# Kernel optimization log

Measured on AMD Instinct MI355X. Metric: run time of the kernel, lower is better.

## Reference

```python
import jax, jax.numpy as jnp
import numpy as np

B, N, D = 32, 1024, 512

def setup_inputs() -> dict:
    key = jax.random.key(0)
    ks = jax.random.split(key, 5)
    s = 1.0 / np.sqrt(D)
    return {
        "x": jax.random.normal(ks[0], (B, N, D), jnp.float32),
        "Wq": jax.random.normal(ks[1], (D, D), jnp.float32) * s,
        "bq": jnp.zeros((D,), jnp.float32),
        "Wk": jax.random.normal(ks[2], (D, D), jnp.float32) * s,
        "bk": jnp.zeros((D,), jnp.float32),
        "Wv": jax.random.normal(ks[3], (D, D), jnp.float32) * s,
        "bv": jnp.zeros((D,), jnp.float32),
        "pos_bias": jax.random.normal(ks[4], (N, N), jnp.float32) * 0.02,
    }

def reference(x, Wq, bq, Wk, bk, Wv, bv, pos_bias):
    # torch nn.Linear: y = x @ W.T + b
    q = x @ Wq.T + bq                      # [B,N,D]
    k = x @ Wk.T + bk                      # [B,N,D]
    v = x @ Wv.T + bv                      # [B,N,D]
    # AFT-full: out[b,t,d] = sig(q)[b,t,d] * sum_s exp(k[b,s,d]+w[t,s]) v[b,s,d]
    #                                        / sum_s exp(k[b,s,d]+w[t,s])
    # exp(k+w) factors as exp(w)*exp(k); the num/den ratio is invariant to
    # per-row shifts of w and per-(b,d) shifts of k, so stabilize both.
    w = pos_bias - jnp.max(pos_bias, axis=1, keepdims=True)   # [T,S]
    kk = k - jnp.max(k, axis=1, keepdims=True)                # [B,S,D]
    ew = jnp.exp(w)
    ek = jnp.exp(kk)
    num = jnp.einsum('ts,bsd->btd', ew, ek * v)               # [B,T,D]
    den = jnp.einsum('ts,bsd->btd', ew, ek)                   # [B,T,D]
    return jax.nn.sigmoid(q) * (num / den)
```

## Files before the change

### kernel.cpp

```cpp
#include <hip/hip_runtime.h>

typedef unsigned short u16;
typedef unsigned int u32;
using frag8 = __attribute__((ext_vector_type(8))) short;
using f32x4 = __attribute__((ext_vector_type(4))) float;

__device__ __forceinline__ u16 f2bf(float f) {
  union { float f; u32 u; } x;
  x.f = f;
  u32 r = (x.u + 0x7fffu + ((x.u >> 16) & 1u)) >> 16;
  return (u16)r;
}

__device__ __forceinline__ void stage_tile(const u16* g, int ld, u16* lds, int tid) {
  const int wv = tid >> 6;
#pragma unroll
  for (int i = 0; i < 2; ++i) {
    const int c = i * 256 + tid;
    const int row = c >> 2;
    const int col = (c & 3) * 8;
    __builtin_amdgcn_global_load_lds(
        (const __attribute__((address_space(1))) void*)(g + (size_t)row * ld + col),
        (__attribute__((address_space(3))) void*)(lds + (size_t)(i * 256 + wv * 64) * 8),
        16, 0, 0);
  }
}

__global__ void conv_kernel(const float* __restrict__ src, u16* __restrict__ dst, int n4) {
  int i = blockIdx.x * 256 + threadIdx.x;
  if (i >= n4) return;
  float4 v = ((const float4*)src)[i];
  ushort4 o;
  o.x = f2bf(v.x); o.y = f2bf(v.y); o.z = f2bf(v.z); o.w = f2bf(v.w);
  ((ushort4*)dst)[i] = o;
}

__global__ void expw_kernel(const float* __restrict__ src, u16* __restrict__ dst, int n4) {
  int i = blockIdx.x * 256 + threadIdx.x;
  if (i >= n4) return;
  float4 v = ((const float4*)src)[i];
  ushort4 o;
  o.x = f2bf(__expf(v.x)); o.y = f2bf(__expf(v.y));
  o.z = f2bf(__expf(v.z)); o.w = f2bf(__expf(v.w));
  ((ushort4*)dst)[i] = o;
}

__global__ __launch_bounds__(256, 3) void q_kernel(const u16* __restrict__ xb,
                                                   const u16* __restrict__ wqb,
                                                   const float* __restrict__ bq,
                                                   float* __restrict__ out) {
  __shared__ __align__(16) u16 As[128 * 32];
  __shared__ __align__(16) u16 Bs[128 * 32];
  const int tid = threadIdx.x;
  const int lane = tid & 63, wv = tid >> 6;
  const int wm = (wv & 1) * 64, wn = (wv >> 1) * 64;
  const int fr = lane & 15, quad = lane >> 4;
  const int m0 = blockIdx.y * 128;
  const int n0 = blockIdx.x * 128;
  f32x4 acc[4][4] = {};
  for (int k0 = 0; k0 < 512; k0 += 32) {
    stage_tile(xb + (size_t)m0 * 512 + k0, 512, As, tid);
    stage_tile(wqb + (size_t)n0 * 512 + k0, 512, Bs, tid);
    __syncthreads();
    frag8 a[4], b[4];
#pragma unroll
    for (int i = 0; i < 4; ++i) a[i] = *(const frag8*)&As[(wm + i * 16 + fr) * 32 + quad * 8];
#pragma unroll
    for (int i = 0; i < 4; ++i) b[i] = *(const frag8*)&Bs[(wn + i * 16 + fr) * 32 + quad * 8];
#pragma unroll
    for (int mi = 0; mi < 4; ++mi)
#pragma unroll
      for (int ni = 0; ni < 4; ++ni)
        acc[mi][ni] = __builtin_amdgcn_mfma_f32_16x16x32_bf16(a[mi], b[ni], acc[mi][ni], 0, 0, 0);
    __syncthreads();
  }
#pragma unroll
  for (int mi = 0; mi < 4; ++mi)
#pragma unroll
    for (int ni = 0; ni < 4; ++ni) {
      const int col = n0 + wn + ni * 16 + fr;
      const float bqv = bq[col];
#pragma unroll
      for (int r = 0; r < 4; ++r) {
        const int row = m0 + wm + mi * 16 + quad * 4 + r;
        const float qv = acc[mi][ni][r] + bqv;
        out[(size_t)row * 512 + col] = 1.0f / (1.0f + __expf(-qv));
      }
    }
}

__global__ __launch_bounds__(256, 2) void kv_kernel(const u16* __restrict__ xb,
                                                    const u16* __restrict__ wkb,
                                                    const u16* __restrict__ wvb,
                                                    const float* __restrict__ bk,
                                                    const float* __restrict__ bv,
                                                    u16* __restrict__ ekT,
                                                    u16* __restrict__ ekvT) {
  __shared__ __align__(16) u16 Ak[128 * 32];
  __shared__ __align__(16) u16 Av[128 * 32];
  __shared__ __align__(16) u16 Bs[128 * 32];
  const int tid = threadIdx.x;
  const int lane = tid & 63, wv = tid >> 6;
  const int wm = (wv & 1) * 64, wn = (wv >> 1) * 64;
  const int fr = lane & 15, quad = lane >> 4;
  const int s0 = blockIdx.x * 128;
  const int d0 = blockIdx.y * 128;
  const int b  = blockIdx.z;
  f32x4 acck[4][4] = {}, accv[4][4] = {};
  for (int k0 = 0; k0 < 512; k0 += 32) {
    stage_tile(wkb + (size_t)d0 * 512 + k0, 512, Ak, tid);
    stage_tile(wvb + (size_t)d0 * 512 + k0, 512, Av, tid);
    stage_tile(xb + ((size_t)b * 1024 + s0) * 512 + k0, 512, Bs, tid);
    __syncthreads();
    frag8 ak[4], av[4], bb[4];
#pragma unroll
    for (int i = 0; i < 4; ++i) {
      ak[i] = *(const frag8*)&Ak[(wm + i * 16 + fr) * 32 + quad * 8];
      av[i] = *(const frag8*)&Av[(wm + i * 16 + fr) * 32 + quad * 8];
      bb[i] = *(const frag8*)&Bs[(wn + i * 16 + fr) * 32 + quad * 8];
    }
#pragma unroll
    for (int mi = 0; mi < 4; ++mi)
#pragma unroll
      for (int ni = 0; ni < 4; ++ni) {
        acck[mi][ni] = __builtin_amdgcn_mfma_f32_16x16x32_bf16(ak[mi], bb[ni], acck[mi][ni], 0, 0, 0);
        accv[mi][ni] = __builtin_amdgcn_mfma_f32_16x16x32_bf16(av[mi], bb[ni], accv[mi][ni], 0, 0, 0);
      }
    __syncthreads();
  }
#pragma unroll
  for (int mi = 0; mi < 4; ++mi)
#pragma unroll
    for (int r = 0; r < 4; ++r) {
      const int d = d0 + wm + mi * 16 + quad * 4 + r;
      const float bkv = bk[d], bvv = bv[d];
#pragma unroll
      for (int ni = 0; ni < 4; ++ni) {
        const int s = s0 + wn + ni * 16 + fr;
        const float ek = __expf(acck[mi][ni][r] + bkv);
        const float vv = accv[mi][ni][r] + bvv;
        const size_t idx = ((size_t)b * 512 + d) * 1024 + s;
        ekT[idx]  = f2bf(ek);
        ekvT[idx] = f2bf(ek * vv);
      }
    }
}

__global__ __launch_bounds__(256, 2) void aft_kernel(const u16* __restrict__ ew,
                                                     const u16* __restrict__ ekT,
                                                     const u16* __restrict__ ekvT,
                                                     float* __restrict__ out) {
  __shared__ __align__(16) u16 As[128 * 32];
  __shared__ __align__(16) u16 B1[128 * 32];
  __shared__ __align__(16) u16 B2[128 * 32];
  const int tid = threadIdx.x;
  const int lane = tid & 63, wv = tid >> 6;
  const int wm = (wv & 1) * 64, wn = (wv >> 1) * 64;
  const int fr = lane & 15, quad = lane >> 4;
  const int d0 = blockIdx.x * 128;
  const int t0 = blockIdx.y * 128;
  const int b  = blockIdx.z;
  f32x4 accn[4][4] = {}, accd[4][4] = {};
  for (int k0 = 0; k0 < 1024; k0 += 32) {
    stage_tile(ew + (size_t)t0 * 1024 + k0, 1024, As, tid);
    stage_tile(ekvT + ((size_t)b * 512 + d0) * 1024 + k0, 1024, B1, tid);
    stage_tile(ekT + ((size_t)b * 512 + d0) * 1024 + k0, 1024, B2, tid);
    __syncthreads();
    frag8 a[4], b1[4], b2[4];
#pragma unroll
    for (int i = 0; i < 4; ++i) {
      a[i]  = *(const frag8*)&As[(wm + i * 16 + fr) * 32 + quad * 8];
      b1[i] = *(const frag8*)&B1[(wn + i * 16 + fr) * 32 + quad * 8];
      b2[i] = *(const frag8*)&B2[(wn + i * 16 + fr) * 32 + quad * 8];
    }
#pragma unroll
    for (int mi = 0; mi < 4; ++mi)
#pragma unroll
      for (int ni = 0; ni < 4; ++ni) {
        accn[mi][ni] = __builtin_amdgcn_mfma_f32_16x16x32_bf16(a[mi], b1[ni], accn[mi][ni], 0, 0, 0);
        accd[mi][ni] = __builtin_amdgcn_mfma_f32_16x16x32_bf16(a[mi], b2[ni], accd[mi][ni], 0, 0, 0);
      }
    __syncthreads();
  }
#pragma unroll
  for (int mi = 0; mi < 4; ++mi)
#pragma unroll
    for (int ni = 0; ni < 4; ++ni)
#pragma unroll
      for (int r = 0; r < 4; ++r) {
        const int t = t0 + wm + mi * 16 + quad * 4 + r;
        const int d = d0 + wn + ni * 16 + fr;
        const size_t idx = ((size_t)b * 1024 + t) * 512 + d;
        const float sq = out[idx];
        out[idx] = sq * accn[mi][ni][r] / accd[mi][ni][r];
      }
}

extern "C" void kernel_launch(void* const* d_in, const int* in_sizes, int n_in,
                              void* d_out, int out_size, void* d_ws, size_t ws_size,
                              hipStream_t stream) {
  const float* x  = (const float*)d_in[0];
  const float* Wq = (const float*)d_in[1];
  const float* bq = (const float*)d_in[2];
  const float* Wk = (const float*)d_in[3];
  const float* bk = (const float*)d_in[4];
  const float* Wv = (const float*)d_in[5];
  const float* bv = (const float*)d_in[6];
  const float* pb = (const float*)d_in[7];
  float* out = (float*)d_out;
  char* ws = (char*)d_ws;
  u16* xb   = (u16*)(ws);
  u16* wqb  = (u16*)(ws + 33554432);
  u16* wkb  = (u16*)(ws + 34078720);
  u16* wvb  = (u16*)(ws + 34603008);
  u16* ewb  = (u16*)(ws + 35127296);
  u16* ekT  = (u16*)(ws + 37224448);
  u16* ekvT = (u16*)(ws + 70778880);

  conv_kernel<<<16384, 256, 0, stream>>>(x, xb, 16777216 / 4);
  conv_kernel<<<256, 256, 0, stream>>>(Wq, wqb, 262144 / 4);
  conv_kernel<<<256, 256, 0, stream>>>(Wk, wkb, 262144 / 4);
  conv_kernel<<<256, 256, 0, stream>>>(Wv, wvb, 262144 / 4);
  expw_kernel<<<1024, 256, 0, stream>>>(pb, ewb, 1048576 / 4);

  q_kernel<<<dim3(4, 256), 256, 0, stream>>>(xb, wqb, bq, out);
  kv_kernel<<<dim3(8, 4, 32), 256, 0, stream>>>(xb, wkb, wvb, bk, bv, ekT, ekvT);
  aft_kernel<<<dim3(4, 8, 32), 256, 0, stream>>>(ewb, ekT, ekvT, out);
}
```

Measured before the change: 294.7 us.

## Double GEMM K-tile to 64 with XOR-swizzled LDS and merge prep kernels

```diff
diff --git a/kernel.cpp b/kernel.cpp
--- a/kernel.cpp
+++ b/kernel.cpp
@@ -12,36 +12,49 @@
   return (u16)r;
 }
 
-__device__ __forceinline__ void stage_tile(const u16* g, int ld, u16* lds, int tid) {
+__device__ __forceinline__ void stage_tile64(const u16* g, int ld, u16* lds, int tid) {
   const int wv = tid >> 6;
 #pragma unroll
-  for (int i = 0; i < 2; ++i) {
+  for (int i = 0; i < 4; ++i) {
     const int c = i * 256 + tid;
-    const int row = c >> 2;
-    const int col = (c & 3) * 8;
+    const int row = c >> 3;
+    const int colc = (c & 7) ^ (row & 7);
     __builtin_amdgcn_global_load_lds(
-        (const __attribute__((address_space(1))) void*)(g + (size_t)row * ld + col),
+        (const __attribute__((address_space(1))) void*)(g + (size_t)row * ld + colc * 8),
         (__attribute__((address_space(3))) void*)(lds + (size_t)(i * 256 + wv * 64) * 8),
         16, 0, 0);
   }
 }
 
-__global__ void conv_kernel(const float* __restrict__ src, u16* __restrict__ dst, int n4) {
-  int i = blockIdx.x * 256 + threadIdx.x;
-  if (i >= n4) return;
+__device__ __forceinline__ frag8 frag_read64(const u16* lds, int row, int kk, int quad) {
+  const int cc = (kk * 4 + quad) ^ (row & 7);
+  return *(const frag8*)&lds[row * 64 + cc * 8];
+}
+
+__global__ void prep_kernel(const float* __restrict__ x, const float* __restrict__ Wq,
+                            const float* __restrict__ Wk, const float* __restrict__ Wv,
+                            const float* __restrict__ pb, u16* __restrict__ xb,
+                            u16* __restrict__ wqb, u16* __restrict__ wkb,
+                            u16* __restrict__ wvb, u16* __restrict__ ewb) {
+  const int blk = blockIdx.x;
+  const float* src;
+  u16* dst;
+  int base;
+  bool ex = false;
+  if (blk < 16384)      { src = x;  dst = xb;  base = blk; }
+  else if (blk < 16640) { src = Wq; dst = wqb; base = blk - 16384; }
+  else if (blk < 16896) { src = Wk; dst = wkb; base = blk - 16640; }
+  else if (blk < 17152) { src = Wv; dst = wvb; base = blk - 16896; }
+  else                  { src = pb; dst = ewb; base = blk - 17152; ex = true; }
+  const int i = base * 256 + threadIdx.x;
   float4 v = ((const float4*)src)[i];
   ushort4 o;
-  o.x = f2bf(v.x); o.y = f2bf(v.y); o.z = f2bf(v.z); o.w = f2bf(v.w);
-  ((ushort4*)dst)[i] = o;
-}
-
-__global__ void expw_kernel(const float* __restrict__ src, u16* __restrict__ dst, int n4) {
-  int i = blockIdx.x * 256 + threadIdx.x;
-  if (i >= n4) return;
-  float4 v = ((const float4*)src)[i];
-  ushort4 o;
-  o.x = f2bf(__expf(v.x)); o.y = f2bf(__expf(v.y));
-  o.z = f2bf(__expf(v.z)); o.w = f2bf(__expf(v.w));
+  if (ex) {
+    o.x = f2bf(__expf(v.x)); o.y = f2bf(__expf(v.y));
+    o.z = f2bf(__expf(v.z)); o.w = f2bf(__expf(v.w));
+  } else {
+    o.x = f2bf(v.x); o.y = f2bf(v.y); o.z = f2bf(v.z); o.w = f2bf(v.w);
+  }
   ((ushort4*)dst)[i] = o;
 }
 
@@ -49,8 +62,8 @@
                                                    const u16* __restrict__ wqb,
                                                    const float* __restrict__ bq,
                                                    float* __restrict__ out) {
-  __shared__ __align__(16) u16 As[128 * 32];
-  __shared__ __align__(16) u16 Bs[128 * 32];
+  __shared__ __align__(16) u16 As[128 * 64];
+  __shared__ __align__(16) u16 Bs[128 * 64];
   const int tid = threadIdx.x;
   const int lane = tid & 63, wv = tid >> 6;
   const int wm = (wv & 1) * 64, wn = (wv >> 1) * 64;
@@ -58,20 +71,24 @@
   const int m0 = blockIdx.y * 128;
   const int n0 = blockIdx.x * 128;
   f32x4 acc[4][4] = {};
-  for (int k0 = 0; k0 < 512; k0 += 32) {
-    stage_tile(xb + (size_t)m0 * 512 + k0, 512, As, tid);
-    stage_tile(wqb + (size_t)n0 * 512 + k0, 512, Bs, tid);
-    __syncthreads();
-    frag8 a[4], b[4];
-#pragma unroll
-    for (int i = 0; i < 4; ++i) a[i] = *(const frag8*)&As[(wm + i * 16 + fr) * 32 + quad * 8];
-#pragma unroll
-    for (int i = 0; i < 4; ++i) b[i] = *(const frag8*)&Bs[(wn + i * 16 + fr) * 32 + quad * 8];
-#pragma unroll
-    for (int mi = 0; mi < 4; ++mi)
-#pragma unroll
-      for (int ni = 0; ni < 4; ++ni)
-        acc[mi][ni] = __builtin_amdgcn_mfma_f32_16x16x32_bf16(a[mi], b[ni], acc[mi][ni], 0, 0, 0);
+  for (int k0 = 0; k0 < 512; k0 += 64) {
+    stage_tile64(xb + (size_t)m0 * 512 + k0, 512, As, tid);
+    stage_tile64(wqb + (size_t)n0 * 512 + k0, 512, Bs, tid);
+    __syncthreads();
+#pragma unroll
+    for (int kk = 0; kk < 2; ++kk) {
+      frag8 a[4], b[4];
+#pragma unroll
+      for (int i = 0; i < 4; ++i) {
+        a[i] = frag_read64(As, wm + i * 16 + fr, kk, quad);
+        b[i] = frag_read64(Bs, wn + i * 16 + fr, kk, quad);
+      }
+#pragma unroll
+      for (int mi = 0; mi < 4; ++mi)
+#pragma unroll
+        for (int ni = 0; ni < 4; ++ni)
+          acc[mi][ni] = __builtin_amdgcn_mfma_f32_16x16x32_bf16(a[mi], b[ni], acc[mi][ni], 0, 0, 0);
+    }
     __syncthreads();
   }
 #pragma unroll
@@ -96,9 +113,9 @@
                                                     const float* __restrict__ bv,
                                                     u16* __restrict__ ekT,
                                                     u16* __restrict__ ekvT) {
-  __shared__ __align__(16) u16 Ak[128 * 32];
-  __shared__ __align__(16) u16 Av[128 * 32];
-  __shared__ __align__(16) u16 Bs[128 * 32];
+  __shared__ __align__(16) u16 Ak[128 * 64];
+  __shared__ __align__(16) u16 Av[128 * 64];
+  __shared__ __align__(16) u16 Bs[128 * 64];
   const int tid = threadIdx.x;
   const int lane = tid & 63, wv = tid >> 6;
   const int wm = (wv & 1) * 64, wn = (wv >> 1) * 64;
@@ -107,25 +124,28 @@
   const int d0 = blockIdx.y * 128;
   const int b  = blockIdx.z;
   f32x4 acck[4][4] = {}, accv[4][4] = {};
-  for (int k0 = 0; k0 < 512; k0 += 32) {
-    stage_tile(wkb + (size_t)d0 * 512 + k0, 512, Ak, tid);
-    stage_tile(wvb + (size_t)d0 * 512 + k0, 512, Av, tid);
-    stage_tile(xb + ((size_t)b * 1024 + s0) * 512 + k0, 512, Bs, tid);
-    __syncthreads();
-    frag8 ak[4], av[4], bb[4];
-#pragma unroll
-    for (int i = 0; i < 4; ++i) {
-      ak[i] = *(const frag8*)&Ak[(wm + i * 16 + fr) * 32 + quad * 8];
-      av[i] = *(const frag8*)&Av[(wm + i * 16 + fr) * 32 + quad * 8];
-      bb[i] = *(const frag8*)&Bs[(wn + i * 16 + fr) * 32 + quad * 8];
-    }
-#pragma unroll
-    for (int mi = 0; mi < 4; ++mi)
-#pragma unroll
-      for (int ni = 0; ni < 4; ++ni) {
-        acck[mi][ni] = __builtin_amdgcn_mfma_f32_16x16x32_bf16(ak[mi], bb[ni], acck[mi][ni], 0, 0, 0);
-        accv[mi][ni] = __builtin_amdgcn_mfma_f32_16x16x32_bf16(av[mi], bb[ni], accv[mi][ni], 0, 0, 0);
-      }
+  for (int k0 = 0; k0 < 512; k0 += 64) {
+    stage_tile64(wkb + (size_t)d0 * 512 + k0, 512, Ak, tid);
+    stage_tile64(wvb + (size_t)d0 * 512 + k0, 512, Av, tid);
+    stage_tile64(xb + ((size_t)b * 1024 + s0) * 512 + k0, 512, Bs, tid);
+    __syncthreads();
+#pragma unroll
+    for (int kk = 0; kk < 2; ++kk) {
+      frag8 ak[4], av[4], bb[4];
+#pragma unroll
+      for (int i = 0; i < 4; ++i) {
+        ak[i] = frag_read64(Ak, wm + i * 16 + fr, kk, quad);
+        av[i] = frag_read64(Av, wm + i * 16 + fr, kk, quad);
+        bb[i] = frag_read64(Bs, wn + i * 16 + fr, kk, quad);
+      }
+#pragma unroll
+      for (int mi = 0; mi < 4; ++mi)
+#pragma unroll
+        for (int ni = 0; ni < 4; ++ni) {
+          acck[mi][ni] = __builtin_amdgcn_mfma_f32_16x16x32_bf16(ak[mi], bb[ni], acck[mi][ni], 0, 0, 0);
+          accv[mi][ni] = __builtin_amdgcn_mfma_f32_16x16x32_bf16(av[mi], bb[ni], accv[mi][ni], 0, 0, 0);
+        }
+    }
     __syncthreads();
   }
 #pragma unroll
@@ -150,9 +170,9 @@
                                                      const u16* __restrict__ ekT,
                                                      const u16* __restrict__ ekvT,
                                                      float* __restrict__ out) {
-  __shared__ __align__(16) u16 As[128 * 32];
-  __shared__ __align__(16) u16 B1[128 * 32];
-  __shared__ __align__(16) u16 B2[128 * 32];
+  __shared__ __align__(16) u16 As[128 * 64];
+  __shared__ __align__(16) u16 B1[128 * 64];
+  __shared__ __align__(16) u16 B2[128 * 64];
   const int tid = threadIdx.x;
   const int lane = tid & 63, wv = tid >> 6;
   const int wm = (wv & 1) * 64, wn = (wv >> 1) * 64;
@@ -161,25 +181,28 @@
   const int t0 = blockIdx.y * 128;
   const int b  = blockIdx.z;
   f32x4 accn[4][4] = {}, accd[4][4] = {};
-  for (int k0 = 0; k0 < 1024; k0 += 32) {
-    stage_tile(ew + (size_t)t0 * 1024 + k0, 1024, As, tid);
-    stage_tile(ekvT + ((size_t)b * 512 + d0) * 1024 + k0, 1024, B1, tid);
-    stage_tile(ekT + ((size_t)b * 512 + d0) * 1024 + k0, 1024, B2, tid);
-    __syncthreads();
-    frag8 a[4], b1[4], b2[4];
-#pragma unroll
-    for (int i = 0; i < 4; ++i) {
-      a[i]  = *(const frag8*)&As[(wm + i * 16 + fr) * 32 + quad * 8];
-      b1[i] = *(const frag8*)&B1[(wn + i * 16 + fr) * 32 + quad * 8];
-      b2[i] = *(const frag8*)&B2[(wn + i * 16 + fr) * 32 + quad * 8];
-    }
-#pragma unroll
-    for (int mi = 0; mi < 4; ++mi)
-#pragma unroll
-      for (int ni = 0; ni < 4; ++ni) {
-        accn[mi][ni] = __builtin_amdgcn_mfma_f32_16x16x32_bf16(a[mi], b1[ni], accn[mi][ni], 0, 0, 0);
-        accd[mi][ni] = __builtin_amdgcn_mfma_f32_16x16x32_bf16(a[mi], b2[ni], accd[mi][ni], 0, 0, 0);
-      }
+  for (int k0 = 0; k0 < 1024; k0 += 64) {
+    stage_tile64(ew + (size_t)t0 * 1024 + k0, 1024, As, tid);
+    stage_tile64(ekvT + ((size_t)b * 512 + d0) * 1024 + k0, 1024, B1, tid);
+    stage_tile64(ekT + ((size_t)b * 512 + d0) * 1024 + k0, 1024, B2, tid);
+    __syncthreads();
+#pragma unroll
+    for (int kk = 0; kk < 2; ++kk) {
+      frag8 a[4], b1[4], b2[4];
+#pragma unroll
+      for (int i = 0; i < 4; ++i) {
+        a[i]  = frag_read64(As, wm + i * 16 + fr, kk, quad);
+        b1[i] = frag_read64(B1, wn + i * 16 + fr, kk, quad);
+        b2[i] = frag_read64(B2, wn + i * 16 + fr, kk, quad);
+      }
+#pragma unroll
+      for (int mi = 0; mi < 4; ++mi)
+#pragma unroll
+        for (int ni = 0; ni < 4; ++ni) {
+          accn[mi][ni] = __builtin_amdgcn_mfma_f32_16x16x32_bf16(a[mi], b1[ni], accn[mi][ni], 0, 0, 0);
+          accd[mi][ni] = __builtin_amdgcn_mfma_f32_16x16x32_bf16(a[mi], b2[ni], accd[mi][ni], 0, 0, 0);
+        }
+    }
     __syncthreads();
   }
 #pragma unroll
@@ -217,12 +240,7 @@
   u16* ekT  = (u16*)(ws + 37224448);
   u16* ekvT = (u16*)(ws + 70778880);
 
-  conv_kernel<<<16384, 256, 0, stream>>>(x, xb, 16777216 / 4);
-  conv_kernel<<<256, 256, 0, stream>>>(Wq, wqb, 262144 / 4);
-  conv_kernel<<<256, 256, 0, stream>>>(Wk, wkb, 262144 / 4);
-  conv_kernel<<<256, 256, 0, stream>>>(Wv, wvb, 262144 / 4);
-  expw_kernel<<<1024, 256, 0, stream>>>(pb, ewb, 1048576 / 4);
-
+  prep_kernel<<<18176, 256, 0, stream>>>(x, Wq, Wk, Wv, pb, xb, wqb, wkb, wvb, ewb);
   q_kernel<<<dim3(4, 256), 256, 0, stream>>>(xb, wqb, bq, out);
   kv_kernel<<<dim3(8, 4, 32), 256, 0, stream>>>(xb, wkb, wvb, bk, bv, ekT, ekvT);
   aft_kernel<<<dim3(4, 8, 32), 256, 0, stream>>>(ewb, ekT, ekvT, out);
```

Measured after the change: 253.6 us. -13.9%, faster.
